# Kernel tuning notes

Hardware: AMD Instinct MI355X
Metric: run time of the kernel (lower is better)

The kernel has to match this reference:

```python
import jax, jax.numpy as jnp
import numpy as np

B_GRAPHS, N2, FDIM, HEADS = 128, 32, 256, 4
TOTAL = 262144


def setup_inputs() -> dict:
    key = jax.random.key(0)
    ks = jax.random.split(key, 6)
    # sorted graph ids, guaranteed to cover all B_GRAPHS values
    batch = jnp.sort(jnp.concatenate([
        jax.random.randint(ks[0], (TOTAL - B_GRAPHS,), 0, B_GRAPHS),
        jnp.arange(B_GRAPHS)])).astype(jnp.int32)
    x = jax.random.normal(ks[1], (TOTAL, FDIM), jnp.float32)
    queries = jax.random.normal(ks[2], (1, N2, FDIM), jnp.float32)
    s = 1.0 / np.sqrt(FDIM)
    in_proj_w = jax.random.uniform(ks[3], (3 * FDIM, FDIM), jnp.float32, -s, s)
    in_proj_b = jnp.zeros((3 * FDIM,), jnp.float32)
    out_proj_w = jax.random.uniform(ks[4], (FDIM, FDIM), jnp.float32, -s, s)
    out_proj_b = jnp.zeros((FDIM,), jnp.float32)
    return {"x": x, "batch": batch, "queries": queries,
            "in_proj_w": in_proj_w, "in_proj_b": in_proj_b,
            "out_proj_w": out_proj_w, "out_proj_b": out_proj_b}


def reference(x, batch, queries, in_proj_w, in_proj_b, out_proj_w, out_proj_b):
    F = x.shape[-1]
    H = HEADS
    d = F // H
    B = int(batch.max()) + 1
    counts = jnp.bincount(batch, length=B)                      # [B]
    N_max = int(counts.max())
    offsets = jnp.concatenate([jnp.zeros((1,), counts.dtype), jnp.cumsum(counts)[:-1]])
    pos = jnp.arange(batch.shape[0]) - offsets[batch]           # position within segment
    # ragged -> padded scatter (equivalent of the python loop)
    x_padded = jnp.zeros((B, N_max, F), x.dtype).at[batch, pos].set(x)
    valid = jnp.arange(N_max)[None, :] < counts[:, None]        # [B, N_max], True = real token

    Wq, Wk, Wv = in_proj_w[:F], in_proj_w[F:2 * F], in_proj_w[2 * F:]
    bq, bk, bv = in_proj_b[:F], in_proj_b[F:2 * F], in_proj_b[2 * F:]

    scale = 1.0 / np.sqrt(d)
    q = (queries[0] @ Wq.T + bq).reshape(N2, H, d) * scale      # [N2, H, d] (shared over B)
    k = (x_padded @ Wk.T + bk).reshape(B, N_max, H, d)
    v = (x_padded @ Wv.T + bv).reshape(B, N_max, H, d)

    scores = jnp.einsum('qhd,bkhd->bhqk', q, k)                 # [B, H, N2, N_max]
    scores = jnp.where(valid[:, None, None, :], scores, -jnp.inf)
    attn = jax.nn.softmax(scores, axis=-1)
    out = jnp.einsum('bhqk,bkhd->bqhd', attn, v).reshape(B, N2, F)
    out = out @ out_proj_w.T + out_proj_b
    return out.reshape(B * N2, F)
```

## Files before the change

kernel.cpp:

```cpp
#include <hip/hip_runtime.h>
#include <hip/hip_bf16.h>

typedef __bf16 bf16x8 __attribute__((ext_vector_type(8)));
typedef float  f32x4  __attribute__((ext_vector_type(4)));

#define MFMA16(a,b,c) __builtin_amdgcn_mfma_f32_16x16x32_bf16((a),(b),(c),0,0,0)

__device__ __forceinline__ unsigned short f2bf(float f){
  unsigned int u = __float_as_uint(f);
  u += 0x7fffu + ((u >> 16) & 1u);
  return (unsigned short)(u >> 16);
}

__device__ __forceinline__ unsigned int cvtpk(float lo, float hi){
  unsigned int r;
  asm("v_cvt_pk_bf16_f32 %0, %1, %2" : "=v"(r) : "v"(lo), "v"(hi));
  return r;
}

__device__ __forceinline__ void block_sync(){
  asm volatile("s_waitcnt lgkmcnt(0)" ::: "memory");
  __builtin_amdgcn_s_barrier();
}

constexpr float SCALE_LOG2E = 0.125f * 1.4426950408889634f;

__global__ void k_prep(const float* __restrict__ queries, const float* __restrict__ ipw,
                       const float* __restrict__ ipb, const float* __restrict__ opw,
                       const float* __restrict__ opb, const int* __restrict__ batch,
                       int total, int* __restrict__ starts,
                       unsigned short* __restrict__ AqF,
                       unsigned short* __restrict__ Cmat, float* __restrict__ cvec)
{
  __shared__ __align__(16) float sh[256];
  __shared__ __align__(16) float sh2[256];
  const int t = threadIdx.x, bid = blockIdx.x;

  if (bid < 32){
    const int q = bid;
    sh[t] = queries[q*256 + t];
    __syncthreads();
    const float* wr = ipw + (size_t)t*256;
    float acc = 0.f;
    #pragma unroll 8
    for (int j = 0; j < 256; j += 4){
      float4 wv = *reinterpret_cast<const float4*>(wr + j);
      float4 qv = *reinterpret_cast<const float4*>(&sh[j]);
      acc += wv.x*qv.x + wv.y*qv.y + wv.z*qv.z + wv.w*qv.w;
    }
    sh2[t] = acc + ipb[t];
    __syncthreads();
    #pragma unroll
    for (int h = 0; h < 4; h++){
      const float* wk = ipw + (size_t)(256 + h*64)*256 + t;
      float a2 = 0.f;
      #pragma unroll 8
      for (int d = 0; d < 64; d++) a2 += sh2[h*64 + d] * wk[(size_t)d*256];
      const int dst = ((h*2 + (q>>4))*8 + (t>>5))*512 + (((t>>3)&3)*16 + (q&15))*8 + (t&7);
      AqF[dst] = f2bf(a2 * SCALE_LOG2E);
    }
  } else if (bid < 288){
    const int g = bid - 32;
    sh[t] = opw[(size_t)g*256 + t];
    __syncthreads();
    #pragma unroll
    for (int h = 0; h < 4; h++){
      const float* wv = ipw + (size_t)(512 + h*64)*256 + t;
      float acc = 0.f;
      #pragma unroll 8
      for (int d = 0; d < 64; d++) acc += wv[(size_t)d*256] * sh[h*64 + d];
      Cmat[(size_t)g*1024 + h*256 + t] = f2bf(acc);
    }
    sh2[t] = ipb[512 + t] * sh[t];
    __syncthreads();
    for (int off = 128; off > 0; off >>= 1){
      if (t < off) sh2[t] += sh2[t + off];
      __syncthreads();
    }
    if (t == 0) cvec[g] = sh2[0] + opb[g];
  } else {
    const int sb = bid - 288;
    const int i0 = sb*1024 + t*4;
    if (i0 + 3 < total){
      if (i0 == 0) starts[0] = 0;
      const int4 b4 = *reinterpret_cast<const int4*>(batch + i0);
      if (b4.y != b4.x) starts[b4.y] = i0 + 1;
      if (b4.z != b4.y) starts[b4.z] = i0 + 2;
      if (b4.w != b4.z) starts[b4.w] = i0 + 3;
      if (i0 + 4 < total){
        const int nxt = batch[i0 + 4];
        if (nxt != b4.w) starts[nxt] = i0 + 4;
      } else {
        starts[128] = total;
      }
    }
  }
}


#define LOADC(dst, c_) { \
  const int c0_ = (c_)*32; \
  _Pragma("unroll") \
  for (int n = 0; n < 4; n++){ \
    const int nl_ = c0_ + nb4 + n; \
    float4 v_ = make_float4(0.f,0.f,0.f,0.f); \
    if (nl_ < cnt) v_ = *reinterpret_cast<const float4*>(xg + (size_t)nl_*256 + fq*4); \
    dst[n] = v_; } }

#define STAGE(xsP, xtP, src) { \
  float fm[4][4]; \
  _Pragma("unroll") \
  for (int n = 0; n < 4; n++){ \
    fm[n][0]=src[n].x; fm[n][1]=src[n].y; fm[n][2]=src[n].z; fm[n][3]=src[n].w; } \
  _Pragma("unroll") \
  for (int n = 0; n < 4; n++){ \
    uint2 w2; w2.x = cvtpk(fm[n][0], fm[n][1]); w2.y = cvtpk(fm[n][2], fm[n][3]); \
    *reinterpret_cast<uint2*>(&(xsP)[(nb4 + n)*264 + fq*4]) = w2; } \
  _Pragma("unroll") \
  for (int j = 0; j < 4; j++){ \
    const int row_ = fq*4 + j; \
    int byte_ = row_*80 + nb4*2; byte_ ^= ((row_>>2)&7)<<4; \
    uint2 w2; w2.x = cvtpk(fm[0][j], fm[1][j]); w2.y = cvtpk(fm[2][j], fm[3][j]); \
    *reinterpret_cast<uint2*>(reinterpret_cast<char*>(xtP) + byte_) = w2; } }

__global__ __launch_bounds__(512, 2) void k_attn(
    const float* __restrict__ x, const int* __restrict__ starts,
    const unsigned short* __restrict__ AqF,
    float* __restrict__ partO, float* __restrict__ partL)
{
  __shared__ __align__(16) unsigned short xsub[2][32*264];
  __shared__ __align__(16) unsigned short xT  [3][256*40];
  __shared__ __align__(16) unsigned short Plds[2][128*40];
  __shared__ __align__(16) float lred[2][128];

  const int tid = threadIdx.x;
  const int wave = tid >> 6, lane = tid & 63, lg = lane >> 4, li = lane & 15;
  const int nb4 = wave*4, fq = lane;
  const int a = wave >> 1, bsel = wave & 1;
  const int colbase = a*32 + li;
  const int bid = blockIdx.x;
  const int g = bid >> 1, s = bid & 1;
  const int s0 = starts[g], s1 = starts[g+1];
  const int cntg = s1 - s0;
  const int half = (cntg + 1) >> 1;
  const int nstart = s0 + s*half;
  int cnt = cntg - s*half; cnt = cnt < 0 ? 0 : (cnt > half ? half : cnt);
  const int chunks = (cnt + 31) >> 5;
  const float* xg = x + (size_t)nstart*256;

  bf16x8 bfragS[2][8];
  #pragma unroll
  for (int rf = 0; rf < 2; rf++){
    const unsigned short* ap = AqF + (size_t)((a*2 + rf)*8)*512 + lane*8;
    #pragma unroll
    for (int kb = 0; kb < 8; kb++)
      bfragS[rf][kb] = *reinterpret_cast<const bf16x8*>(ap + kb*512);
  }

  f32x4 oacc[16];
  #pragma unroll
  for (int i = 0; i < 16; i++) oacc[i] = f32x4{0.f,0.f,0.f,0.f};
  float lsum0 = 0.f, lsum1 = 0.f;

  int bvb0 = (wave*32 + li)*80 + lg*16;      bvb0 ^= (((wave*32 + li)>>2)&7)<<4;
  int bvb1 = (wave*32 + 16 + li)*80 + lg*16; bvb1 ^= (((wave*32 + 16 + li)>>2)&7)<<4;

  float4 rA[4], rB[4];
  if (chunks > 0){
    LOADC(rA, 0);
    if (chunks > 1) LOADC(rB, 1);
    STAGE(xsub[0], xT[0], rA);
    if (chunks > 2) LOADC(rA, 2);
    block_sync();
  }

  int cur3 = 0;
  for (int c = 0; c < chunks; ++c){
    const int cur2 = c & 1;
    const int nxt3 = (cur3 == 2) ? 0 : cur3 + 1;
    if (c + 1 < chunks){
      unsigned short* xsP = xsub[cur2 ^ 1];
      unsigned short* xtP = xT[nxt3];
      if (c & 1){ STAGE(xsP, xtP, rA); if (c + 3 < chunks) LOADC(rA, c + 3); }
      else      { STAGE(xsP, xtP, rB); if (c + 3 < chunks) LOADC(rB, c + 3); }
    }

    f32x4 sc0 = f32x4{0.f,0.f,0.f,0.f}, sc1 = f32x4{0.f,0.f,0.f,0.f};
    #pragma unroll
    for (int kb = 0; kb < 8; kb++){
      const bf16x8 af = *reinterpret_cast<const bf16x8*>(&xsub[cur2][(bsel*16 + li)*264 + kb*32 + lg*8]);
      sc0 = MFMA16(af, bfragS[0][kb], sc0);
      sc1 = MFMA16(af, bfragS[1][kb], sc1);
    }

    const int nodebase = c*32 + bsel*16 + lg*4;
    float p0[4], p1[4];
    #pragma unroll
    for (int r = 0; r < 4; r++){
      const bool v = (nodebase + r) < cnt;
      p0[r] = v ? __builtin_exp2f(sc0[r]) : 0.f;
      p1[r] = v ? __builtin_exp2f(sc1[r]) : 0.f;
      lsum0 += p0[r]; lsum1 += p1[r];
    }
    {
      char* pl = reinterpret_cast<char*>(&Plds[cur2][0]);
      uint2 w0; w0.x = cvtpk(p0[0], p0[1]); w0.y = cvtpk(p0[2], p0[3]);
      uint2 w1; w1.x = cvtpk(p1[0], p1[1]); w1.y = cvtpk(p1[2], p1[3]);
      *reinterpret_cast<uint2*>(pl + colbase*80        + bsel*32 + lg*8) = w0;
      *reinterpret_cast<uint2*>(pl + (colbase+16)*80   + bsel*32 + lg*8) = w1;
    }

    block_sync();

    const char* xtC = reinterpret_cast<const char*>(xT[cur3]);
    const bf16x8 bv0 = *reinterpret_cast<const bf16x8*>(xtC + bvb0);
    const bf16x8 bv1 = *reinterpret_cast<const bf16x8*>(xtC + bvb1);
    #pragma unroll
    for (int rt = 0; rt < 8; rt++){
      const bf16x8 pa = *reinterpret_cast<const bf16x8*>(&Plds[cur2][(rt*16 + li)*40 + lg*8]);
      oacc[rt*2]   = MFMA16(pa, bv0, oacc[rt*2]);
      oacc[rt*2+1] = MFMA16(pa, bv1, oacc[rt*2+1]);
    }
    cur3 = nxt3;
  }

  lsum0 += __shfl_xor(lsum0, 16); lsum0 += __shfl_xor(lsum0, 32);
  lsum1 += __shfl_xor(lsum1, 16); lsum1 += __shfl_xor(lsum1, 32);
  if (lane < 16){
    lred[bsel][colbase]      = lsum0;
    lred[bsel][colbase + 16] = lsum1;
  }
  block_sync();
  const int pbase = bid*128;
  if (tid < 128) partL[pbase + tid] = lred[0][tid] + lred[1][tid];

  #pragma unroll
  for (int rt = 0; rt < 8; rt++){
    #pragma unroll
    for (int r = 0; r < 4; r++){
      const size_t orow = (size_t)(pbase + rt*16 + lg*4 + r)*256;
      partO[orow + wave*32 + li]      = oacc[rt*2][r];
      partO[orow + wave*32 + 16 + li] = oacc[rt*2+1][r];
    }
  }
}

__global__ __launch_bounds__(512, 1) void k_out(
    const float* __restrict__ partO, const float* __restrict__ partL,
    const unsigned short* __restrict__ Cmat, const float* __restrict__ cvec,
    float* __restrict__ out)
{
  __shared__ __align__(16) unsigned short plds[16*1024];
  __shared__ float sinv[64];
  const int tid = threadIdx.x;
  const int g = blockIdx.x >> 1, qh = blockIdx.x & 1;
  const int p0 = 2*g, p1 = 2*g + 1;
  if (tid < 64){
    const int h = tid >> 4, qr = tid & 15;
    const int row = h*32 + qh*16 + qr;
    const float L = partL[p0*128 + row] + partL[p1*128 + row];
    sinv[tid] = 1.f / L;
  }
  __syncthreads();
  #pragma unroll
  for (int i = 0; i < 8; i++){
    const int idx = tid + i*512;
    const int qr = idx >> 8;
    const int cg = idx & 255;
    const int h = cg >> 6, f4 = (cg & 63)*4;
    const int row = h*32 + qh*16 + qr;
    const float4 o0 = *reinterpret_cast<const float4*>(&partO[(size_t)(p0*128 + row)*256 + f4]);
    const float4 o1 = *reinterpret_cast<const float4*>(&partO[(size_t)(p1*128 + row)*256 + f4]);
    const float sc = sinv[h*16 + qr];
    uint2 w; w.x = cvtpk((o0.x+o1.x)*sc, (o0.y+o1.y)*sc);
             w.y = cvtpk((o0.z+o1.z)*sc, (o0.w+o1.w)*sc);
    const int col4 = cg*4;
    const int bc = (col4*2) ^ ((qr & 7) << 4);
    *reinterpret_cast<uint2*>(reinterpret_cast<char*>(plds) + qr*2048 + bc) = w;
  }
  __syncthreads();
  const int wave = tid >> 6, lane = tid & 63, lg = lane >> 4, li = lane & 15;
  f32x4 acc0 = {0.f,0.f,0.f,0.f}, acc1 = {0.f,0.f,0.f,0.f};
  const float cv0 = cvec[wave*32 + li], cv1 = cvec[wave*32 + 16 + li];
  const unsigned short* cb0 = Cmat + (size_t)(wave*32 + li)*1024;
  const unsigned short* cb1 = Cmat + (size_t)(wave*32 + 16 + li)*1024;
  #pragma unroll 8
  for (int kb = 0; kb < 32; kb++){
    const int bc = ((kb*32 + lg*8)*2) ^ ((li & 7) << 4);
    const bf16x8 aa = *reinterpret_cast<const bf16x8*>(reinterpret_cast<const char*>(plds) + li*2048 + bc);
    const bf16x8 b0 = *reinterpret_cast<const bf16x8*>(cb0 + kb*32 + lg*8);
    const bf16x8 b1 = *reinterpret_cast<const bf16x8*>(cb1 + kb*32 + lg*8);
    acc0 = MFMA16(aa, b0, acc0);
    acc1 = MFMA16(aa, b1, acc1);
  }
  #pragma unroll
  for (int r = 0; r < 4; r++){
    const int q = lg*4 + r;
    const size_t orow = (size_t)(g*32 + qh*16 + q)*256;
    out[orow + wave*32 + li]      = acc0[r] + cv0;
    out[orow + wave*32 + 16 + li] = acc1[r] + cv1;
  }
}


extern "C" void kernel_launch(void* const* d_in, const int* in_sizes, int n_in,
                              void* d_out, int out_size, void* d_ws, size_t ws_size,
                              hipStream_t stream)
{
  const float* x       = (const float*)d_in[0];
  const int*   batch   = (const int*)d_in[1];
  const float* queries = (const float*)d_in[2];
  const float* ipw     = (const float*)d_in[3];
  const float* ipb     = (const float*)d_in[4];
  const float* opw     = (const float*)d_in[5];
  const float* opb     = (const float*)d_in[6];
  float* out = (float*)d_out;
  const int total = in_sizes[1];

  char* w = (char*)d_ws;
  int*            starts = (int*)(w);
  unsigned short* AqF    = (unsigned short*)(w + 36*1024);
  unsigned short* Cmat   = (unsigned short*)(w + 102*1024);
  float*          cvec   = (float*)(w + 616*1024);
  float*          partO  = (float*)(w + (size_t)1024*1024);
  float*          partL  = (float*)(w + (size_t)1024*1024 + (size_t)256*128*256*4);

  k_prep<<<544, 256, 0, stream>>>(queries, ipw, ipb, opw, opb, batch, total,
                                  starts, AqF, Cmat, cvec);
  k_attn<<<256, 512, 0, stream>>>(x, starts, AqF, partO, partL);
  k_out<<<256, 512, 0, stream>>>(partO, partL, Cmat, cvec, out);
}
```

Baseline: 113.8 us.

## Double k_attn block to 1024 threads with half per-wave work and swizzled P

```diff
diff --git a/kernel.cpp b/kernel.cpp
--- a/kernel.cpp
+++ b/kernel.cpp
@@ -98,32 +98,25 @@
 }
 
 
-#define LOADC(dst, c_) { \
+#define LOADC(c_) { \
   const int c0_ = (c_)*32; \
   _Pragma("unroll") \
   for (int n = 0; n < 4; n++){ \
-    const int nl_ = c0_ + nb4 + n; \
-    float4 v_ = make_float4(0.f,0.f,0.f,0.f); \
-    if (nl_ < cnt) v_ = *reinterpret_cast<const float4*>(xg + (size_t)nl_*256 + fq*4); \
-    dst[n] = v_; } }
-
-#define STAGE(xsP, xtP, src) { \
-  float fm[4][4]; \
+    int nl_ = c0_ + nq*4 + n; nl_ = nl_ < cnt-1 ? nl_ : cnt-1; \
+    rA[n] = *reinterpret_cast<const float2*>(xg + (size_t)nl_*256 + fp*2); } }
+
+#define STAGE(xsP, xtP) { \
   _Pragma("unroll") \
-  for (int n = 0; n < 4; n++){ \
-    fm[n][0]=src[n].x; fm[n][1]=src[n].y; fm[n][2]=src[n].z; fm[n][3]=src[n].w; } \
-  _Pragma("unroll") \
-  for (int n = 0; n < 4; n++){ \
-    uint2 w2; w2.x = cvtpk(fm[n][0], fm[n][1]); w2.y = cvtpk(fm[n][2], fm[n][3]); \
-    *reinterpret_cast<uint2*>(&(xsP)[(nb4 + n)*264 + fq*4]) = w2; } \
-  _Pragma("unroll") \
-  for (int j = 0; j < 4; j++){ \
-    const int row_ = fq*4 + j; \
-    int byte_ = row_*80 + nb4*2; byte_ ^= ((row_>>2)&7)<<4; \
-    uint2 w2; w2.x = cvtpk(fm[0][j], fm[1][j]); w2.y = cvtpk(fm[2][j], fm[3][j]); \
-    *reinterpret_cast<uint2*>(reinterpret_cast<char*>(xtP) + byte_) = w2; } }
-
-__global__ __launch_bounds__(512, 2) void k_attn(
+  for (int n = 0; n < 4; n++) \
+    *reinterpret_cast<unsigned int*>(&(xsP)[(nq*4 + n)*264 + fp*2]) = cvtpk(rA[n].x, rA[n].y); \
+  { const int f0_ = fp*2; \
+    uint2 w0_; w0_.x = cvtpk(rA[0].x, rA[1].x); w0_.y = cvtpk(rA[2].x, rA[3].x); \
+    *reinterpret_cast<uint2*>(reinterpret_cast<char*>(xtP) + ((f0_*80 + nq*8) ^ (((f0_>>2)&7)<<4))) = w0_; \
+    const int f1_ = fp*2 + 1; \
+    uint2 w1_; w1_.x = cvtpk(rA[0].y, rA[1].y); w1_.y = cvtpk(rA[2].y, rA[3].y); \
+    *reinterpret_cast<uint2*>(reinterpret_cast<char*>(xtP) + ((f1_*80 + nq*8) ^ (((f1_>>2)&7)<<4))) = w1_; } }
+
+__global__ __launch_bounds__(1024, 4) void k_attn(
     const float* __restrict__ x, const int* __restrict__ starts,
     const unsigned short* __restrict__ AqF,
     float* __restrict__ partO, float* __restrict__ partL)
@@ -135,9 +128,9 @@
 
   const int tid = threadIdx.x;
   const int wave = tid >> 6, lane = tid & 63, lg = lane >> 4, li = lane & 15;
-  const int nb4 = wave*4, fq = lane;
-  const int a = wave >> 1, bsel = wave & 1;
-  const int colbase = a*32 + li;
+  const int rg = wave >> 1, bsel = wave & 1;
+  const int fs = wave * 16;
+  const int nq = tid >> 7, fp = tid & 127;
   const int bid = blockIdx.x;
   const int g = bid >> 1, s = bid & 1;
   const int s0 = starts[g], s1 = starts[g+1];
@@ -148,29 +141,21 @@
   const int chunks = (cnt + 31) >> 5;
   const float* xg = x + (size_t)nstart*256;
 
-  bf16x8 bfragS[2][8];
-  #pragma unroll
-  for (int rf = 0; rf < 2; rf++){
-    const unsigned short* ap = AqF + (size_t)((a*2 + rf)*8)*512 + lane*8;
-    #pragma unroll
-    for (int kb = 0; kb < 8; kb++)
-      bfragS[rf][kb] = *reinterpret_cast<const bf16x8*>(ap + kb*512);
-  }
-
-  f32x4 oacc[16];
-  #pragma unroll
-  for (int i = 0; i < 16; i++) oacc[i] = f32x4{0.f,0.f,0.f,0.f};
-  float lsum0 = 0.f, lsum1 = 0.f;
-
-  int bvb0 = (wave*32 + li)*80 + lg*16;      bvb0 ^= (((wave*32 + li)>>2)&7)<<4;
-  int bvb1 = (wave*32 + 16 + li)*80 + lg*16; bvb1 ^= (((wave*32 + 16 + li)>>2)&7)<<4;
-
-  float4 rA[4], rB[4];
+  bf16x8 bfragS[8];
+  #pragma unroll
+  for (int kb = 0; kb < 8; kb++)
+    bfragS[kb] = *reinterpret_cast<const bf16x8*>(AqF + (size_t)(rg*8 + kb)*512 + lane*8);
+
+  f32x4 oacc[8];
+  #pragma unroll
+  for (int i = 0; i < 8; i++) oacc[i] = f32x4{0.f,0.f,0.f,0.f};
+  float rsum = 0.f;
+
+  float2 rA[4];
   if (chunks > 0){
-    LOADC(rA, 0);
-    if (chunks > 1) LOADC(rB, 1);
-    STAGE(xsub[0], xT[0], rA);
-    if (chunks > 2) LOADC(rA, 2);
+    LOADC(0);
+    STAGE(xsub[0], xT[0]);
+    if (chunks > 1) LOADC(1);
     block_sync();
   }
 
@@ -178,58 +163,55 @@
   for (int c = 0; c < chunks; ++c){
     const int cur2 = c & 1;
     const int nxt3 = (cur3 == 2) ? 0 : cur3 + 1;
-    if (c + 1 < chunks){
-      unsigned short* xsP = xsub[cur2 ^ 1];
-      unsigned short* xtP = xT[nxt3];
-      if (c & 1){ STAGE(xsP, xtP, rA); if (c + 3 < chunks) LOADC(rA, c + 3); }
-      else      { STAGE(xsP, xtP, rB); if (c + 3 < chunks) LOADC(rB, c + 3); }
-    }
-
-    f32x4 sc0 = f32x4{0.f,0.f,0.f,0.f}, sc1 = f32x4{0.f,0.f,0.f,0.f};
+
+    f32x4 sacc = f32x4{0.f,0.f,0.f,0.f};
+    __builtin_amdgcn_s_setprio(1);
     #pragma unroll
     for (int kb = 0; kb < 8; kb++){
       const bf16x8 af = *reinterpret_cast<const bf16x8*>(&xsub[cur2][(bsel*16 + li)*264 + kb*32 + lg*8]);
-      sc0 = MFMA16(af, bfragS[0][kb], sc0);
-      sc1 = MFMA16(af, bfragS[1][kb], sc1);
-    }
+      sacc = MFMA16(af, bfragS[kb], sacc);
+    }
+    __builtin_amdgcn_s_setprio(0);
 
     const int nodebase = c*32 + bsel*16 + lg*4;
-    float p0[4], p1[4];
+    float p[4];
     #pragma unroll
     for (int r = 0; r < 4; r++){
-      const bool v = (nodebase + r) < cnt;
-      p0[r] = v ? __builtin_exp2f(sc0[r]) : 0.f;
-      p1[r] = v ? __builtin_exp2f(sc1[r]) : 0.f;
-      lsum0 += p0[r]; lsum1 += p1[r];
+      p[r] = (nodebase + r < cnt) ? __builtin_exp2f(sacc[r]) : 0.f;
+      rsum += p[r];
     }
     {
-      char* pl = reinterpret_cast<char*>(&Plds[cur2][0]);
-      uint2 w0; w0.x = cvtpk(p0[0], p0[1]); w0.y = cvtpk(p0[2], p0[3]);
-      uint2 w1; w1.x = cvtpk(p1[0], p1[1]); w1.y = cvtpk(p1[2], p1[3]);
-      *reinterpret_cast<uint2*>(pl + colbase*80        + bsel*32 + lg*8) = w0;
-      *reinterpret_cast<uint2*>(pl + (colbase+16)*80   + bsel*32 + lg*8) = w1;
+      const int row = rg*16 + li;
+      uint2 w; w.x = cvtpk(p[0], p[1]); w.y = cvtpk(p[2], p[3]);
+      *reinterpret_cast<uint2*>(reinterpret_cast<char*>(Plds[cur2])
+          + ((row*80 + bsel*32 + lg*8) ^ (((row>>2)&7)<<4))) = w;
+    }
+
+    if (c + 1 < chunks){
+      STAGE(xsub[cur2 ^ 1], xT[nxt3]);
+      if (c + 2 < chunks) LOADC(c + 2);
     }
 
     block_sync();
 
     const char* xtC = reinterpret_cast<const char*>(xT[cur3]);
-    const bf16x8 bv0 = *reinterpret_cast<const bf16x8*>(xtC + bvb0);
-    const bf16x8 bv1 = *reinterpret_cast<const bf16x8*>(xtC + bvb1);
+    const int fr = fs + li;
+    const bf16x8 bv = *reinterpret_cast<const bf16x8*>(xtC + (((fr*80 + lg*16)) ^ (((fr>>2)&7)<<4)));
+    const char* plC = reinterpret_cast<const char*>(Plds[cur2]);
+    __builtin_amdgcn_s_setprio(1);
     #pragma unroll
     for (int rt = 0; rt < 8; rt++){
-      const bf16x8 pa = *reinterpret_cast<const bf16x8*>(&Plds[cur2][(rt*16 + li)*40 + lg*8]);
-      oacc[rt*2]   = MFMA16(pa, bv0, oacc[rt*2]);
-      oacc[rt*2+1] = MFMA16(pa, bv1, oacc[rt*2+1]);
-    }
+      const int prow = rt*16 + li;
+      const bf16x8 pa = *reinterpret_cast<const bf16x8*>(plC + (((prow*80 + lg*16)) ^ (((prow>>2)&7)<<4)));
+      oacc[rt] = MFMA16(pa, bv, oacc[rt]);
+    }
+    __builtin_amdgcn_s_setprio(0);
     cur3 = nxt3;
   }
 
-  lsum0 += __shfl_xor(lsum0, 16); lsum0 += __shfl_xor(lsum0, 32);
-  lsum1 += __shfl_xor(lsum1, 16); lsum1 += __shfl_xor(lsum1, 32);
-  if (lane < 16){
-    lred[bsel][colbase]      = lsum0;
-    lred[bsel][colbase + 16] = lsum1;
-  }
+  rsum += __shfl_xor(rsum, 16);
+  rsum += __shfl_xor(rsum, 32);
+  if (lane < 16) lred[bsel][rg*16 + li] = rsum;
   block_sync();
   const int pbase = bid*128;
   if (tid < 128) partL[pbase + tid] = lred[0][tid] + lred[1][tid];
@@ -238,9 +220,7 @@
   for (int rt = 0; rt < 8; rt++){
     #pragma unroll
     for (int r = 0; r < 4; r++){
-      const size_t orow = (size_t)(pbase + rt*16 + lg*4 + r)*256;
-      partO[orow + wave*32 + li]      = oacc[rt*2][r];
-      partO[orow + wave*32 + 16 + li] = oacc[rt*2+1][r];
+      partO[(size_t)(pbase + rt*16 + lg*4 + r)*256 + fs + li] = oacc[rt][r];
     }
   }
 }
@@ -327,6 +307,6 @@
 
   k_prep<<<544, 256, 0, stream>>>(queries, ipw, ipb, opw, opb, batch, total,
                                   starts, AqF, Cmat, cvec);
-  k_attn<<<256, 512, 0, stream>>>(x, starts, AqF, partO, partL);
+  k_attn<<<256, 1024, 0, stream>>>(x, starts, AqF, partO, partL);
   k_out<<<256, 512, 0, stream>>>(partO, partL, Cmat, cvec, out);
 }
```

After: 114.4 us. No clear change (+0.6%).
